# Kernel optimization log

Measured on AMD Instinct MI355X. Metric: run time of the kernel, lower is better.

## Reference

```python
import jax, jax.numpy as jnp
import numpy as np

B, T, DIM = 4, 2048, 512
HEADS, HD = 8, 64
RANK = 256
WIN = 256
EPS = 1e-6
ROPE_BASE = 10000.0


def _rope_tables(seq_len, head_dim):
    pos = jnp.arange(seq_len, dtype=jnp.float32)                      # [T]
    inv_freq = 1.0 / (ROPE_BASE ** (jnp.arange(0, head_dim, 2, dtype=jnp.float32) / head_dim))  # [HD/2]
    ang = pos[:, None] * inv_freq[None, :]                            # [T, HD/2]
    cos = jnp.concatenate([jnp.cos(ang), jnp.cos(ang)], axis=-1)      # [T, HD]
    sin = jnp.concatenate([jnp.sin(ang), jnp.sin(ang)], axis=-1)
    return cos, sin


def _rotate_half(x):
    x1, x2 = jnp.split(x, 2, axis=-1)
    return jnp.concatenate([-x2, x1], axis=-1)


def _apply_rope(q, k):
    # q, k: [B, H, T, HD]
    cos, sin = _rope_tables(q.shape[2], q.shape[3])
    cos = cos[None, None]; sin = sin[None, None]
    q = q * cos + _rotate_half(q) * sin
    k = k * cos + _rotate_half(k) * sin
    return q, k


def _rmsnorm(x, w):
    x32 = x.astype(jnp.float32)
    n = x32 * jax.lax.rsqrt(jnp.mean(x32 * x32, axis=-1, keepdims=True) + EPS)
    return n.astype(x.dtype) * w


def setup_inputs() -> dict:
    key = jax.random.key(0)
    ks = jax.random.split(key, 6)
    s = 0.02
    return {
        "x": jax.random.normal(ks[0], (B, T, DIM), dtype=jnp.float32),
        "Wq": jax.random.normal(ks[1], (DIM, DIM), dtype=jnp.float32) * s,
        "Wkv_down": jax.random.normal(ks[2], (RANK, DIM), dtype=jnp.float32) * s,
        "kv_norm_w": jnp.ones((RANK,), dtype=jnp.float32),
        "Wkv_up": jax.random.normal(ks[3], (2 * DIM, RANK), dtype=jnp.float32) * s,
        "Wout": jax.random.normal(ks[4], (DIM, DIM), dtype=jnp.float32) * s,
    }


def reference(x, Wq, Wkv_down, kv_norm_w, Wkv_up, Wout):
    # q projection -> [B, H, T, HD]
    q = jnp.einsum('btd,ed->bte', x, Wq).reshape(B, T, HEADS, HD).transpose(0, 2, 1, 3)
    # latent KV: down-proj -> RMSNorm -> up-proj
    c_kv = jnp.einsum('btd,rd->btr', x, Wkv_down)          # [B, T, RANK]
    c_kv = _rmsnorm(c_kv, kv_norm_w)
    kv = jnp.einsum('btr,er->bte', c_kv, Wkv_up)            # [B, T, 2*DIM]
    kv = kv.reshape(B, T, 2, HEADS, HD).transpose(2, 0, 3, 1, 4)
    k, v = kv[0], kv[1]                                     # [B, H, T, HD]
    q, k = _apply_rope(q, k)
    rows = jnp.arange(T)[:, None]
    cols = jnp.arange(T)[None, :]
    mask = jnp.abs(cols - rows) <= WIN                      # [T, T]
    scale = HD ** -0.5
    scores = jnp.einsum('bhtd,bhsd->bhts', q, k) * scale    # [B, H, T, T]
    scores = jnp.where(mask[None, None], scores, jnp.float32(-jnp.inf))
    attn = jax.nn.softmax(scores, axis=-1)
    out = jnp.einsum('bhts,bhsd->bhtd', attn, v)            # [B, H, T, HD]
    out = out.transpose(0, 2, 1, 3).reshape(B, T, DIM)
    return jnp.einsum('btd,ed->bte', out, Wout)
```

## Files before the change

### kernel.cpp

```cpp
#include <hip/hip_runtime.h>
#include <math.h>

#define BB 4
#define TT 2048
#define DIMM 512
#define HEADS 8
#define HDIM 64
#define RANKK 256
#define WINN 256

static constexpr int BT = BB * TT;
#define SC2 0.1803368801111244f

typedef short bf8_t __attribute__((ext_vector_type(8)));
typedef float f32x4 __attribute__((ext_vector_type(4)));

__device__ __forceinline__ unsigned short f2bf(float f) {
    unsigned u = __float_as_uint(f);
    u += 0x7fffu + ((u >> 16) & 1u);
    return (unsigned short)(u >> 16);
}
__device__ __forceinline__ float bf2f(unsigned short u) {
    return __uint_as_float(((unsigned)u) << 16);
}

typedef __attribute__((address_space(1))) void gvoid_t;
typedef __attribute__((address_space(3))) void lvoid_t;
__device__ __forceinline__ void gload16(const void* g, void* l) {
    __builtin_amdgcn_global_load_lds((gvoid_t*)g, (lvoid_t*)l, 16, 0, 0);
}
#define WAIT_VM0_BARRIER() do { \
    asm volatile("s_waitcnt vmcnt(0)" ::: "memory"); \
    __builtin_amdgcn_s_barrier(); \
    __builtin_amdgcn_sched_barrier(0); \
} while (0)

__device__ __forceinline__ void cvt4(const float* __restrict__ s,
                                     unsigned short* __restrict__ d, int i) {
    float4 v = *reinterpret_cast<const float4*>(s + i);
    *reinterpret_cast<ushort4*>(d + i) =
        make_ushort4(f2bf(v.x), f2bf(v.y), f2bf(v.z), f2bf(v.w));
}

__global__ __launch_bounds__(256) void prep_kernel(
    const float* __restrict__ x, const float* __restrict__ Wq,
    const float* __restrict__ Wkd, const float* __restrict__ Wku,
    const float* __restrict__ wn, const float* __restrict__ Wout,
    unsigned short* __restrict__ xb, unsigned short* __restrict__ wcomb,
    unsigned short* __restrict__ wkub, unsigned short* __restrict__ woutb,
    float* __restrict__ cosT, float* __restrict__ sinT) {
    int bid = blockIdx.x;
    if (bid < 4096) {
        cvt4(x, xb, (bid * 256 + threadIdx.x) * 4);
    } else if (bid < 4352) {
        cvt4(Wq, wcomb, ((bid - 4096) * 256 + threadIdx.x) * 4);
    } else if (bid < 4480) {
        cvt4(Wkd, wcomb + DIMM * DIMM, ((bid - 4352) * 256 + threadIdx.x) * 4);
    } else if (bid < 4736) {
        int i = ((bid - 4480) * 256 + threadIdx.x) * 4;
        float4 v = *reinterpret_cast<const float4*>(Wku + i);
        float4 s = *reinterpret_cast<const float4*>(wn + (i & 255));
        *reinterpret_cast<ushort4*>(wkub + i) =
            make_ushort4(f2bf(v.x * s.x), f2bf(v.y * s.y), f2bf(v.z * s.z), f2bf(v.w * s.w));
    } else if (bid < 4992) {
        cvt4(Wout, woutb, ((bid - 4736) * 256 + threadIdx.x) * 4);
    } else {
        int idx = (bid - 4992) * 256 + threadIdx.x;
        int t = idx >> 5, f = idx & 31;
        double freq = pow(10000.0, -(double)f / 32.0);
        double ang = (double)t * freq;
        cosT[idx] = (float)cos(ang);
        sinT[idx] = (float)sin(ang);
    }
}

__global__ __launch_bounds__(256) void rinv_kernel(const unsigned short* __restrict__ ckvb0,
                                                   float* __restrict__ rinv) {
    int row = blockIdx.x * 4 + (threadIdx.x >> 6);
    int lane = threadIdx.x & 63;
    ushort4 v4 = *reinterpret_cast<const ushort4*>(ckvb0 + (size_t)row * 256 + lane * 4);
    float x0 = bf2f(v4.x), x1 = bf2f(v4.y), x2 = bf2f(v4.z), x3 = bf2f(v4.w);
    float ss = x0 * x0 + x1 * x1 + x2 * x2 + x3 * x3;
#pragma unroll
    for (int off = 32; off > 0; off >>= 1) ss += __shfl_xor(ss, off);
    if (lane == 0) rinv[row] = rsqrtf(ss * (1.0f / RANKK) + 1e-6f);
}

template<int MODE>
__global__ __launch_bounds__(512) void gemm_bf(const unsigned short* __restrict__ A,
                                               const unsigned short* __restrict__ W,
                                               float* __restrict__ Cf,
                                               unsigned short* __restrict__ O1,
                                               unsigned short* __restrict__ O2,
                                               const float* __restrict__ cosT,
                                               const float* __restrict__ sinT,
                                               const float* __restrict__ rinvp,
                                               int K, int N) {
    __shared__ __align__(16) unsigned short As[2][128 * 64];
    __shared__ __align__(16) unsigned short Ws[2][128 * 64];
    const int tid = threadIdx.x;
    const int lane = tid & 63, w = tid >> 6;
    const int lr = lane & 15, hi = lane >> 4;
    const int m0 = blockIdx.x * 128, n0 = blockIdx.y * 128;
    const int wr = (w >> 1) * 32, wc = (w & 1) * 64;
    const int ar1 = tid >> 3;
    const int ac1 = ((tid & 7) ^ (ar1 & 7)) << 3;
    const int ar2 = ar1 + 64;

    f32x4 acc[2][4];
#pragma unroll
    for (int i = 0; i < 2; ++i)
#pragma unroll
        for (int j = 0; j < 4; ++j) acc[i][j] = 0.0f;

    const int NT = K >> 6;
    auto stage = [&](int t, int b) {
        const int kt = t * 64;
        gload16(A + (size_t)(m0 + ar1) * K + kt + ac1, &As[b][tid * 8]);
        gload16(A + (size_t)(m0 + ar2) * K + kt + ac1, &As[b][(tid + 512) * 8]);
        gload16(W + (size_t)(n0 + ar1) * K + kt + ac1, &Ws[b][tid * 8]);
        gload16(W + (size_t)(n0 + ar2) * K + kt + ac1, &Ws[b][(tid + 512) * 8]);
    };

    stage(0, 0);
    WAIT_VM0_BARRIER();
    for (int t = 0; t < NT; ++t) {
        const int cur = t & 1;
        if (t + 1 < NT) stage(t + 1, cur ^ 1);
        bf8_t af[2][2], bw[4][2];
#pragma unroll
        for (int i = 0; i < 2; ++i) {
            int row = wr + i * 16 + lr;
#pragma unroll
            for (int kk = 0; kk < 2; ++kk)
                af[i][kk] = *reinterpret_cast<const bf8_t*>(
                    &As[cur][row * 64 + (((kk * 4 + hi) ^ (row & 7)) << 3)]);
        }
#pragma unroll
        for (int j = 0; j < 4; ++j) {
            int row = wc + j * 16 + lr;
#pragma unroll
            for (int kk = 0; kk < 2; ++kk)
                bw[j][kk] = *reinterpret_cast<const bf8_t*>(
                    &Ws[cur][row * 64 + (((kk * 4 + hi) ^ (row & 7)) << 3)]);
        }
#pragma unroll
        for (int kk = 0; kk < 2; ++kk)
#pragma unroll
            for (int i = 0; i < 2; ++i)
#pragma unroll
                for (int j = 0; j < 4; ++j)
                    acc[i][j] = __builtin_amdgcn_mfma_f32_16x16x32_bf16(af[i][kk], bw[j][kk], acc[i][j], 0, 0, 0);
        if (t + 1 < NT) WAIT_VM0_BARRIER();
    }

    if constexpr (MODE == 0) {
#pragma unroll
        for (int i = 0; i < 2; ++i)
#pragma unroll
            for (int j = 0; j < 4; ++j)
#pragma unroll
                for (int r = 0; r < 4; ++r)
                    Cf[(size_t)(m0 + wr + i * 16 + 4 * hi + r) * N + n0 + wc + j * 16 + lr] = acc[i][j][r];
    } else if (n0 < 512) {
        int h = (n0 + wc) >> 6;
#pragma unroll
        for (int i = 0; i < 2; ++i) {
            int tb = m0 + wr + i * 16 + 4 * hi;
            float4 rv4 = make_float4(1.f, 1.f, 1.f, 1.f);
            if constexpr (MODE == 2) rv4 = *reinterpret_cast<const float4*>(rinvp + tb);
#pragma unroll
            for (int j = 0; j < 2; ++j)
#pragma unroll
                for (int r = 0; r < 4; ++r) {
                    int t = tb + r;
                    int b = t >> 11, tt = t & 2047;
                    int ff = j * 16 + lr;
                    float rv = (&rv4.x)[r];
                    float x1 = acc[i][j][r] * rv, x2 = acc[i][j + 2][r] * rv;
                    float cc = cosT[tt * 32 + ff], ss = sinT[tt * 32 + ff];
                    unsigned short* dp = O1 + ((size_t)((b * 8 + h) * 2048 + tt)) * 64;
                    dp[ff]      = f2bf(x1 * cc - x2 * ss);
                    dp[ff + 32] = f2bf(x2 * cc + x1 * ss);
                }
        }
    } else if constexpr (MODE == 1) {
        int cb = n0 - 512 + wc;
#pragma unroll
        for (int i = 0; i < 2; ++i)
#pragma unroll
            for (int j = 0; j < 4; ++j)
#pragma unroll
                for (int r = 0; r < 4; ++r)
                    O2[(size_t)(m0 + wr + i * 16 + 4 * hi + r) * 256 + cb + j * 16 + lr] = f2bf(acc[i][j][r]);
    } else {
        int cb = n0 + wc - 512;
        int h = cb >> 6;
#pragma unroll
        for (int i = 0; i < 2; ++i) {
            int tb = m0 + wr + i * 16 + 4 * hi;
            int b = tb >> 11, tt = tb & 2047;
            float4 rv4 = *reinterpret_cast<const float4*>(rinvp + tb);
#pragma unroll
            for (int j = 0; j < 4; ++j) {
                int hd = j * 16 + lr;
                ushort4 o = make_ushort4(f2bf(acc[i][j][0] * rv4.x), f2bf(acc[i][j][1] * rv4.y),
                                         f2bf(acc[i][j][2] * rv4.z), f2bf(acc[i][j][3] * rv4.w));
                *reinterpret_cast<ushort4*>(O2 + (((size_t)(b * 8 + h) * 64 + hd) * 2048 + tt)) = o;
            }
        }
    }
}

__global__ __launch_bounds__(512) void attn_mfma(const unsigned short* __restrict__ qbf,
                                                 const unsigned short* __restrict__ kbf,
                                                 const unsigned short* __restrict__ vT,
                                                 unsigned short* __restrict__ aob) {
    __shared__ __align__(16) unsigned short Kl[2][64 * 64];
    __shared__ __align__(16) unsigned short Vl[2][64 * 64];
    __shared__ unsigned short Pl[128][72];
    const int tid = threadIdx.x;
    const int lane = tid & 63, w = tid >> 6;
    const int lr = lane & 15, hi = lane >> 4;

    const int fid = blockIdx.x;
    const int swz = (fid & 7) * 64 + (fid >> 3);
    const int t0 = (swz & 15) * 128;
    const int bh = swz >> 4;

    const unsigned short* qp = qbf + ((size_t)bh * TT + t0 + w * 16 + lr) * HDIM;
    bf8_t qa[2];
    qa[0] = *reinterpret_cast<const bf8_t*>(qp + hi * 8);
    qa[1] = *reinterpret_cast<const bf8_t*>(qp + 32 + hi * 8);

    f32x4 oc[4];
#pragma unroll
    for (int f = 0; f < 4; ++f) oc[f] = 0.0f;
    float lp[4] = {0.f, 0.f, 0.f, 0.f};

    const int smin = max(0, t0 - WINN);
    const int smax = min(TT, t0 + 128 + WINN);
    const int NT = (smax - smin) >> 6;

    const int st_row = tid >> 3;
    const int st_c = tid & 7;
    const int st_cs = (st_c ^ (st_row & 7)) << 3;

    auto stage = [&](int t, int b) {
        const int s0 = smin + t * 64;
        gload16(kbf + ((size_t)bh * TT + s0 + st_row) * HDIM + st_cs, &Kl[b][tid * 8]);
        gload16(vT + ((size_t)bh * 64 + st_row) * TT + s0 + st_cs, &Vl[b][tid * 8]);
    };

    stage(0, 0);
    WAIT_VM0_BARRIER();
    for (int t = 0; t < NT; ++t) {
        const int cur = t & 1;
        if (t + 1 < NT) stage(t + 1, cur ^ 1);
        const int s0 = smin + t * 64;

        f32x4 sacc[4];
#pragma unroll
        for (int f = 0; f < 4; ++f) sacc[f] = 0.0f;
        __builtin_amdgcn_s_setprio(1);
#pragma unroll
        for (int ks = 0; ks < 2; ++ks)
#pragma unroll
            for (int f = 0; f < 4; ++f) {
                int row = f * 16 + lr;
                bf8_t kb = *reinterpret_cast<const bf8_t*>(
                    &Kl[cur][row * 64 + (((ks * 4 + hi) ^ (row & 7)) << 3)]);
                sacc[f] = __builtin_amdgcn_mfma_f32_16x16x32_bf16(qa[ks], kb, sacc[f], 0, 0, 0);
            }
        __builtin_amdgcn_s_setprio(0);

        const int off_w = s0 - t0 - w * 16;
        const bool edge = (off_w + 63 > WINN) || (off_w - 15 < -WINN);
#pragma unroll
        for (int f = 0; f < 4; ++f)
#pragma unroll
            for (int r = 0; r < 4; ++r) {
                float p;
                if (edge) {
                    int d = off_w + f * 16 + lr - 4 * hi - r;
                    p = (d <= WINN && d >= -WINN) ? exp2f(sacc[f][r] * SC2) : 0.f;
                } else {
                    p = exp2f(sacc[f][r] * SC2);
                }
                lp[r] += p;
                Pl[w * 16 + 4 * hi + r][f * 16 + lr] = f2bf(p);
            }

        __builtin_amdgcn_s_setprio(1);
#pragma unroll
        for (int ks = 0; ks < 2; ++ks) {
            bf8_t pa = *reinterpret_cast<const bf8_t*>(&Pl[w * 16 + lr][ks * 32 + hi * 8]);
#pragma unroll
            for (int f = 0; f < 4; ++f) {
                int row = f * 16 + lr;
                bf8_t vb = *reinterpret_cast<const bf8_t*>(
                    &Vl[cur][row * 64 + (((ks * 4 + hi) ^ (row & 7)) << 3)]);
                oc[f] = __builtin_amdgcn_mfma_f32_16x16x32_bf16(pa, vb, oc[f], 0, 0, 0);
            }
        }
        __builtin_amdgcn_s_setprio(0);
        if (t + 1 < NT) WAIT_VM0_BARRIER();
    }

#pragma unroll
    for (int r = 0; r < 4; ++r) {
        lp[r] += __shfl_xor(lp[r], 1);
        lp[r] += __shfl_xor(lp[r], 2);
        lp[r] += __shfl_xor(lp[r], 4);
        lp[r] += __shfl_xor(lp[r], 8);
    }

    int b = bh >> 3, h = bh & 7;
#pragma unroll
    for (int r = 0; r < 4; ++r) {
        float inv = 1.0f / lp[r];
        int t = t0 + w * 16 + 4 * hi + r;
        unsigned short* op = aob + ((size_t)b * TT + t) * DIMM + h * HDIM;
#pragma unroll
        for (int f = 0; f < 4; ++f)
            op[f * 16 + lr] = f2bf(oc[f][r] * inv);
    }
}

extern "C" void kernel_launch(void* const* d_in, const int* in_sizes, int n_in,
                              void* d_out, int out_size, void* d_ws, size_t ws_size,
                              hipStream_t stream) {
    const float* x     = (const float*)d_in[0];
    const float* Wq    = (const float*)d_in[1];
    const float* Wkd   = (const float*)d_in[2];
    const float* wnorm = (const float*)d_in[3];
    const float* Wku   = (const float*)d_in[4];
    const float* Wout  = (const float*)d_in[5];
    float* out = (float*)d_out;
    char* ws = (char*)d_ws;

    unsigned short* xb    = (unsigned short*)(ws + 0);
    unsigned short* qb    = (unsigned short*)(ws + 8388608);
    unsigned short* kb    = (unsigned short*)(ws + 16777216);
    unsigned short* vTb   = (unsigned short*)(ws + 25165824);
    unsigned short* ckvb0 = (unsigned short*)(ws + 33554432);
    unsigned short* aob   = (unsigned short*)(ws + 37748736);
    unsigned short* wcomb = (unsigned short*)(ws + 46137344);
    unsigned short* wkub  = (unsigned short*)(ws + 46923776);
    unsigned short* woutb = (unsigned short*)(ws + 47448064);
    float*          rinvb = (float*)(ws + 47972352);
    float*          cosT  = (float*)(ws + 48005120);
    float*          sinT  = (float*)(ws + 48267264);

    prep_kernel<<<5248, 256, 0, stream>>>(x, Wq, Wkd, Wku, wnorm, Wout,
                                          xb, wcomb, wkub, woutb, cosT, sinT);

    gemm_bf<1><<<dim3(BT / 128, 6), 512, 0, stream>>>(xb, wcomb, nullptr, qb, ckvb0,
                                                      cosT, sinT, nullptr, DIMM, 768);
    rinv_kernel<<<BT / 4, 256, 0, stream>>>(ckvb0, rinvb);

    gemm_bf<2><<<dim3(BT / 128, 8), 512, 0, stream>>>(ckvb0, wkub, nullptr, kb, vTb,
                                                      cosT, sinT, rinvb, RANKK, 1024);

    attn_mfma<<<512, 512, 0, stream>>>(qb, kb, vTb, aob);

    gemm_bf<0><<<dim3(BT / 128, 4), 512, 0, stream>>>(aob, woutb, out, nullptr, nullptr,
                                                      nullptr, nullptr, nullptr, DIMM, DIMM);
}
```

Measured before the change: 77.92 us.

## Fuse RMS sum-of-squares into GEMM epilogue, use packed bf16 converts, shrink out-proj tile

The separate rinv kernel is removed. The first GEMM now writes per-row partial sums of squares for the latent KV, and the second GEMM combines them into the RMS scale. Float-to-bf16 conversions throughout switch to the packed v_cvt_pk_bf16_f32 instruction. The output-projection GEMM is templated on tile height and uses 64-row tiles with 256 threads, giving more blocks. This saves a launch and a reread of c_kv. The hardware convert uses its own rounding and NaN handling, and the partial sums are taken from fp32 accumulators rather than from the bf16-rounded values the old kernel read.

```diff
diff --git a/kernel.cpp b/kernel.cpp
--- a/kernel.cpp
+++ b/kernel.cpp
@@ -20,8 +20,10 @@
     u += 0x7fffu + ((u >> 16) & 1u);
     return (unsigned short)(u >> 16);
 }
-__device__ __forceinline__ float bf2f(unsigned short u) {
-    return __uint_as_float(((unsigned)u) << 16);
+__device__ __forceinline__ unsigned f2bf2(float a, float b) {
+    unsigned r;
+    asm("v_cvt_pk_bf16_f32 %0, %1, %2" : "=v"(r) : "v"(a), "v"(b));
+    return r;
 }
 
 typedef __attribute__((address_space(1))) void gvoid_t;
@@ -38,8 +40,8 @@
 __device__ __forceinline__ void cvt4(const float* __restrict__ s,
                                      unsigned short* __restrict__ d, int i) {
     float4 v = *reinterpret_cast<const float4*>(s + i);
-    *reinterpret_cast<ushort4*>(d + i) =
-        make_ushort4(f2bf(v.x), f2bf(v.y), f2bf(v.z), f2bf(v.w));
+    uint2 st = make_uint2(f2bf2(v.x, v.y), f2bf2(v.z, v.w));
+    *reinterpret_cast<uint2*>(d + i) = st;
 }
 
 __global__ __launch_bounds__(256) void prep_kernel(
@@ -60,8 +62,8 @@
         int i = ((bid - 4480) * 256 + threadIdx.x) * 4;
         float4 v = *reinterpret_cast<const float4*>(Wku + i);
         float4 s = *reinterpret_cast<const float4*>(wn + (i & 255));
-        *reinterpret_cast<ushort4*>(wkub + i) =
-            make_ushort4(f2bf(v.x * s.x), f2bf(v.y * s.y), f2bf(v.z * s.z), f2bf(v.w * s.w));
+        uint2 st = make_uint2(f2bf2(v.x * s.x, v.y * s.y), f2bf2(v.z * s.z, v.w * s.w));
+        *reinterpret_cast<uint2*>(wkub + i) = st;
     } else if (bid < 4992) {
         cvt4(Wout, woutb, ((bid - 4736) * 256 + threadIdx.x) * 4);
     } else {
@@ -74,38 +76,23 @@
     }
 }
 
-__global__ __launch_bounds__(256) void rinv_kernel(const unsigned short* __restrict__ ckvb0,
-                                                   float* __restrict__ rinv) {
-    int row = blockIdx.x * 4 + (threadIdx.x >> 6);
-    int lane = threadIdx.x & 63;
-    ushort4 v4 = *reinterpret_cast<const ushort4*>(ckvb0 + (size_t)row * 256 + lane * 4);
-    float x0 = bf2f(v4.x), x1 = bf2f(v4.y), x2 = bf2f(v4.z), x3 = bf2f(v4.w);
-    float ss = x0 * x0 + x1 * x1 + x2 * x2 + x3 * x3;
-#pragma unroll
-    for (int off = 32; off > 0; off >>= 1) ss += __shfl_xor(ss, off);
-    if (lane == 0) rinv[row] = rsqrtf(ss * (1.0f / RANKK) + 1e-6f);
-}
-
-template<int MODE>
-__global__ __launch_bounds__(512) void gemm_bf(const unsigned short* __restrict__ A,
-                                               const unsigned short* __restrict__ W,
-                                               float* __restrict__ Cf,
-                                               unsigned short* __restrict__ O1,
-                                               unsigned short* __restrict__ O2,
-                                               const float* __restrict__ cosT,
-                                               const float* __restrict__ sinT,
-                                               const float* __restrict__ rinvp,
-                                               int K, int N) {
-    __shared__ __align__(16) unsigned short As[2][128 * 64];
+template<int MODE, int BM>
+__global__ __launch_bounds__(BM * 4) void gemm_bf(const unsigned short* __restrict__ A,
+                                                  const unsigned short* __restrict__ W,
+                                                  float* __restrict__ Cf,
+                                                  unsigned short* __restrict__ O1,
+                                                  unsigned short* __restrict__ O2,
+                                                  const float* __restrict__ cosT,
+                                                  const float* __restrict__ sinT,
+                                                  float* __restrict__ ssum,
+                                                  int K, int N) {
+    __shared__ __align__(16) unsigned short As[2][BM * 64];
     __shared__ __align__(16) unsigned short Ws[2][128 * 64];
     const int tid = threadIdx.x;
     const int lane = tid & 63, w = tid >> 6;
     const int lr = lane & 15, hi = lane >> 4;
-    const int m0 = blockIdx.x * 128, n0 = blockIdx.y * 128;
+    const int m0 = blockIdx.x * BM, n0 = blockIdx.y * 128;
     const int wr = (w >> 1) * 32, wc = (w & 1) * 64;
-    const int ar1 = tid >> 3;
-    const int ac1 = ((tid & 7) ^ (ar1 & 7)) << 3;
-    const int ar2 = ar1 + 64;
 
     f32x4 acc[2][4];
 #pragma unroll
@@ -116,10 +103,16 @@
     const int NT = K >> 6;
     auto stage = [&](int t, int b) {
         const int kt = t * 64;
-        gload16(A + (size_t)(m0 + ar1) * K + kt + ac1, &As[b][tid * 8]);
-        gload16(A + (size_t)(m0 + ar2) * K + kt + ac1, &As[b][(tid + 512) * 8]);
-        gload16(W + (size_t)(n0 + ar1) * K + kt + ac1, &Ws[b][tid * 8]);
-        gload16(W + (size_t)(n0 + ar2) * K + kt + ac1, &Ws[b][(tid + 512) * 8]);
+#pragma unroll
+        for (int c = tid; c < BM * 8; c += BM * 4) {
+            int row = c >> 3, sc = ((c & 7) ^ (row & 7)) << 3;
+            gload16(A + (size_t)(m0 + row) * K + kt + sc, &As[b][c * 8]);
+        }
+#pragma unroll
+        for (int c = tid; c < 1024; c += BM * 4) {
+            int row = c >> 3, sc = ((c & 7) ^ (row & 7)) << 3;
+            gload16(W + (size_t)(n0 + row) * K + kt + sc, &Ws[b][c * 8]);
+        }
     };
 
     stage(0, 0);
@@ -168,7 +161,16 @@
         for (int i = 0; i < 2; ++i) {
             int tb = m0 + wr + i * 16 + 4 * hi;
             float4 rv4 = make_float4(1.f, 1.f, 1.f, 1.f);
-            if constexpr (MODE == 2) rv4 = *reinterpret_cast<const float4*>(rinvp + tb);
+            if constexpr (MODE == 2) {
+                float4 sa = *reinterpret_cast<const float4*>(ssum + tb);
+                float4 sb = *reinterpret_cast<const float4*>(ssum + 8192 + tb);
+                float4 sc = *reinterpret_cast<const float4*>(ssum + 16384 + tb);
+                float4 sd = *reinterpret_cast<const float4*>(ssum + 24576 + tb);
+                rv4.x = rsqrtf((sa.x + sb.x + sc.x + sd.x) * (1.0f / RANKK) + 1e-6f);
+                rv4.y = rsqrtf((sa.y + sb.y + sc.y + sd.y) * (1.0f / RANKK) + 1e-6f);
+                rv4.z = rsqrtf((sa.z + sb.z + sc.z + sd.z) * (1.0f / RANKK) + 1e-6f);
+                rv4.w = rsqrtf((sa.w + sb.w + sc.w + sd.w) * (1.0f / RANKK) + 1e-6f);
+            }
 #pragma unroll
             for (int j = 0; j < 2; ++j)
 #pragma unroll
@@ -179,20 +181,39 @@
                     float rv = (&rv4.x)[r];
                     float x1 = acc[i][j][r] * rv, x2 = acc[i][j + 2][r] * rv;
                     float cc = cosT[tt * 32 + ff], ss = sinT[tt * 32 + ff];
+                    unsigned u = f2bf2(x1 * cc - x2 * ss, x2 * cc + x1 * ss);
                     unsigned short* dp = O1 + ((size_t)((b * 8 + h) * 2048 + tt)) * 64;
-                    dp[ff]      = f2bf(x1 * cc - x2 * ss);
-                    dp[ff + 32] = f2bf(x2 * cc + x1 * ss);
+                    dp[ff]      = (unsigned short)u;
+                    dp[ff + 32] = (unsigned short)(u >> 16);
                 }
         }
     } else if constexpr (MODE == 1) {
         int cb = n0 - 512 + wc;
-#pragma unroll
-        for (int i = 0; i < 2; ++i)
-#pragma unroll
-            for (int j = 0; j < 4; ++j)
-#pragma unroll
-                for (int r = 0; r < 4; ++r)
-                    O2[(size_t)(m0 + wr + i * 16 + 4 * hi + r) * 256 + cb + j * 16 + lr] = f2bf(acc[i][j][r]);
+        int part = ((n0 - 512) >> 7) * 2 + (w & 1);
+#pragma unroll
+        for (int i = 0; i < 2; ++i) {
+            int tb = m0 + wr + i * 16 + 4 * hi;
+#pragma unroll
+            for (int r = 0; r < 4; ++r) {
+                float ps = acc[i][0][r] * acc[i][0][r] + acc[i][1][r] * acc[i][1][r]
+                         + acc[i][2][r] * acc[i][2][r] + acc[i][3][r] * acc[i][3][r];
+                ps += __shfl_xor(ps, 1);
+                ps += __shfl_xor(ps, 2);
+                ps += __shfl_xor(ps, 4);
+                ps += __shfl_xor(ps, 8);
+                if (lr == 0) ssum[part * 8192 + tb + r] = ps;
+            }
+#pragma unroll
+            for (int j = 0; j < 4; ++j) {
+                unsigned a01 = f2bf2(acc[i][j][0], acc[i][j][1]);
+                unsigned a23 = f2bf2(acc[i][j][2], acc[i][j][3]);
+                unsigned short* dp = O2 + (size_t)tb * 256 + cb + j * 16 + lr;
+                dp[0]   = (unsigned short)a01;
+                dp[256] = (unsigned short)(a01 >> 16);
+                dp[512] = (unsigned short)a23;
+                dp[768] = (unsigned short)(a23 >> 16);
+            }
+        }
     } else {
         int cb = n0 + wc - 512;
         int h = cb >> 6;
@@ -200,13 +221,21 @@
         for (int i = 0; i < 2; ++i) {
             int tb = m0 + wr + i * 16 + 4 * hi;
             int b = tb >> 11, tt = tb & 2047;
-            float4 rv4 = *reinterpret_cast<const float4*>(rinvp + tb);
+            float4 sa = *reinterpret_cast<const float4*>(ssum + tb);
+            float4 sb = *reinterpret_cast<const float4*>(ssum + 8192 + tb);
+            float4 sc = *reinterpret_cast<const float4*>(ssum + 16384 + tb);
+            float4 sd = *reinterpret_cast<const float4*>(ssum + 24576 + tb);
+            float4 rv4;
+            rv4.x = rsqrtf((sa.x + sb.x + sc.x + sd.x) * (1.0f / RANKK) + 1e-6f);
+            rv4.y = rsqrtf((sa.y + sb.y + sc.y + sd.y) * (1.0f / RANKK) + 1e-6f);
+            rv4.z = rsqrtf((sa.z + sb.z + sc.z + sd.z) * (1.0f / RANKK) + 1e-6f);
+            rv4.w = rsqrtf((sa.w + sb.w + sc.w + sd.w) * (1.0f / RANKK) + 1e-6f);
 #pragma unroll
             for (int j = 0; j < 4; ++j) {
                 int hd = j * 16 + lr;
-                ushort4 o = make_ushort4(f2bf(acc[i][j][0] * rv4.x), f2bf(acc[i][j][1] * rv4.y),
-                                         f2bf(acc[i][j][2] * rv4.z), f2bf(acc[i][j][3] * rv4.w));
-                *reinterpret_cast<ushort4*>(O2 + (((size_t)(b * 8 + h) * 64 + hd) * 2048 + tt)) = o;
+                uint2 st = make_uint2(f2bf2(acc[i][j][0] * rv4.x, acc[i][j][1] * rv4.y),
+                                      f2bf2(acc[i][j][2] * rv4.z, acc[i][j][3] * rv4.w));
+                *reinterpret_cast<uint2*>(O2 + (((size_t)(b * 8 + h) * 64 + hd) * 2048 + tt)) = st;
             }
         }
     }
@@ -277,19 +306,28 @@
         const int off_w = s0 - t0 - w * 16;
         const bool edge = (off_w + 63 > WINN) || (off_w - 15 < -WINN);
 #pragma unroll
-        for (int f = 0; f < 4; ++f)
+        for (int f = 0; f < 4; ++f) {
+            float p[4];
 #pragma unroll
             for (int r = 0; r < 4; ++r) {
-                float p;
+                float v;
                 if (edge) {
                     int d = off_w + f * 16 + lr - 4 * hi - r;
-                    p = (d <= WINN && d >= -WINN) ? exp2f(sacc[f][r] * SC2) : 0.f;
+                    v = (d <= WINN && d >= -WINN) ? exp2f(sacc[f][r] * SC2) : 0.f;
                 } else {
-                    p = exp2f(sacc[f][r] * SC2);
+                    v = exp2f(sacc[f][r] * SC2);
                 }
-                lp[r] += p;
-                Pl[w * 16 + 4 * hi + r][f * 16 + lr] = f2bf(p);
-            }
+                p[r] = v;
+                lp[r] += v;
+            }
+            unsigned a01 = f2bf2(p[0], p[1]);
+            unsigned a23 = f2bf2(p[2], p[3]);
+            unsigned short* bp = &Pl[w * 16 + 4 * hi][f * 16 + lr];
+            bp[0]   = (unsigned short)a01;
+            bp[72]  = (unsigned short)(a01 >> 16);
+            bp[144] = (unsigned short)a23;
+            bp[216] = (unsigned short)(a23 >> 16);
+        }
 
         __builtin_amdgcn_s_setprio(1);
 #pragma unroll
@@ -321,9 +359,12 @@
         float inv = 1.0f / lp[r];
         int t = t0 + w * 16 + 4 * hi + r;
         unsigned short* op = aob + ((size_t)b * TT + t) * DIMM + h * HDIM;
-#pragma unroll
-        for (int f = 0; f < 4; ++f)
-            op[f * 16 + lr] = f2bf(oc[f][r] * inv);
+        unsigned u0 = f2bf2(oc[0][r] * inv, oc[1][r] * inv);
+        unsigned u1 = f2bf2(oc[2][r] * inv, oc[3][r] * inv);
+        op[lr]      = (unsigned short)u0;
+        op[16 + lr] = (unsigned short)(u0 >> 16);
+        op[32 + lr] = (unsigned short)u1;
+        op[48 + lr] = (unsigned short)(u1 >> 16);
     }
 }
 
@@ -348,22 +389,21 @@
     unsigned short* wcomb = (unsigned short*)(ws + 46137344);
     unsigned short* wkub  = (unsigned short*)(ws + 46923776);
     unsigned short* woutb = (unsigned short*)(ws + 47448064);
-    float*          rinvb = (float*)(ws + 47972352);
     float*          cosT  = (float*)(ws + 48005120);
     float*          sinT  = (float*)(ws + 48267264);
+    float*          ssum  = (float*)(ws + 48529408);
 
     prep_kernel<<<5248, 256, 0, stream>>>(x, Wq, Wkd, Wku, wnorm, Wout,
                                           xb, wcomb, wkub, woutb, cosT, sinT);
 
-    gemm_bf<1><<<dim3(BT / 128, 6), 512, 0, stream>>>(xb, wcomb, nullptr, qb, ckvb0,
-                                                      cosT, sinT, nullptr, DIMM, 768);
-    rinv_kernel<<<BT / 4, 256, 0, stream>>>(ckvb0, rinvb);
-
-    gemm_bf<2><<<dim3(BT / 128, 8), 512, 0, stream>>>(ckvb0, wkub, nullptr, kb, vTb,
-                                                      cosT, sinT, rinvb, RANKK, 1024);
+    gemm_bf<1, 128><<<dim3(BT / 128, 6), 512, 0, stream>>>(xb, wcomb, nullptr, qb, ckvb0,
+                                                           cosT, sinT, ssum, DIMM, 768);
+
+    gemm_bf<2, 128><<<dim3(BT / 128, 8), 512, 0, stream>>>(ckvb0, wkub, nullptr, kb, vTb,
+                                                           cosT, sinT, ssum, RANKK, 1024);
 
     attn_mfma<<<512, 512, 0, stream>>>(qb, kb, vTb, aob);
 
-    gemm_bf<0><<<dim3(BT / 128, 4), 512, 0, stream>>>(aob, woutb, out, nullptr, nullptr,
-                                                      nullptr, nullptr, nullptr, DIMM, DIMM);
-}
+    gemm_bf<0, 64><<<dim3(BT / 64, 4), 256, 0, stream>>>(aob, woutb, out, nullptr, nullptr,
+                                                         nullptr, nullptr, nullptr, DIMM, DIMM);
+}
```

Result: faster. 73.75 us (-5.3%).
